# Optimization experiments

Measured on AMD Instinct MI355X. Metric: run time of the kernel, lower is better.

## Reference

```python
import jax, jax.numpy as jnp
import numpy as np

N, F, H, K, O = 16384, 64, 128, 16, 10


def setup_inputs() -> dict:
    key = jax.random.key(0)
    ks = jax.random.split(key, 12)
    s = lambda fan: 1.0 / np.sqrt(fan)
    return {
        "x": jax.random.normal(ks[0], (N, F), dtype=jnp.float32),
        "edge_index": jax.random.randint(ks[1], (2, N * 8), 0, N),  # unused by forward
        "mlp_w1": jax.random.normal(ks[2], (2 * F, H), dtype=jnp.float32) * s(2 * F),
        "mlp_b1": jnp.zeros((H,), jnp.float32),
        "mlp_w2": jax.random.normal(ks[3], (H, H), dtype=jnp.float32) * s(H),
        "mlp_b2": jnp.zeros((H,), jnp.float32),
        "gcn_w": jax.random.normal(ks[4], (H, H), dtype=jnp.float32) * s(H),
        "gcn_b": jnp.zeros((H,), jnp.float32),
        "gnn_out_w": jax.random.normal(ks[5], (H, H), dtype=jnp.float32) * s(H),
        "gnn_out_b": jnp.zeros((H,), jnp.float32),
        "out_w": jax.random.normal(ks[6], (H, O), dtype=jnp.float32) * s(H),
        "out_b": jnp.zeros((O,), jnp.float32),
        "k": K,
    }


def _forward(x, mlp_w1, mlp_b1, mlp_w2, mlp_b2, gcn_w, gcn_b,
             gnn_out_w, gnn_out_b, out_w, out_b, k):
    n = x.shape[0]
    # ---- dynamic kNN graph in feature space (includes self, dist 0) ----
    sq = jnp.sum(x * x, axis=-1)                       # [N]
    d2 = sq[:, None] + sq[None, :] - 2.0 * (x @ x.T)   # [N,N] squared dists
    _, idx = jax.lax.top_k(-d2, k)                     # [N,k] neighbor (source) ids per query
    # ---- EdgeConv message: MLP(cat(x_i, x_j - x_i)), max-aggregate over k ----
    x_j = x[idx]                                       # [N,k,F]
    x_i = jnp.broadcast_to(x[:, None, :], x_j.shape)   # [N,k,F]
    m = jnp.concatenate([x_i, x_j - x_i], axis=-1)     # [N,k,2F]
    m = jax.nn.relu(m @ mlp_w1 + mlp_b1)
    m = jax.nn.log_softmax(m @ mlp_w2 + mlp_b2, axis=-1)
    h = jnp.max(m, axis=1)                             # [N,H] max aggregation
    # ---- GCNConv on the kNN edge_index (+ self loops, symmetric norm) ----
    loop = jnp.arange(n)
    src = jnp.concatenate([idx.reshape(-1), loop])     # sources (x_j)
    dst = jnp.concatenate([jnp.repeat(loop, k), loop]) # targets (x_i)
    deg = jax.ops.segment_sum(jnp.ones_like(src, h.dtype), dst, num_segments=n)
    dinv = jax.lax.rsqrt(jnp.maximum(deg, 1.0))
    norm = dinv[src] * dinv[dst]                       # [E]
    hw = h @ gcn_w                                     # [N,H]
    h = jax.ops.segment_sum(norm[:, None] * hw[src], dst, num_segments=n) + gcn_b
    # ---- inner GNN output head (Linear + Softmax) ----
    h = jax.nn.softmax(h @ gnn_out_w + gnn_out_b, axis=-1)
    # ---- GNN_Combo output head (Linear + Softmax) ----
    return jax.nn.softmax(h @ out_w + out_b, axis=-1)  # [N,O]


def reference(x, edge_index, mlp_w1, mlp_b1, mlp_w2, mlp_b2, gcn_w, gcn_b,
              gnn_out_w, gnn_out_b, out_w, out_b, k):
    # edge_index is accepted by GNN_Combo.forward but unused (kNN graph replaces it)
    del edge_index
    return _forward(x, mlp_w1, mlp_b1, mlp_w2, mlp_b2, gcn_w, gcn_b,
                    gnn_out_w, gnn_out_b, out_w, out_b, k)
```

## Files before the change

kernel.cpp:

```cpp
#include <hip/hip_runtime.h>
#include <hip/hip_fp16.h>
#include <cfloat>
#include <cmath>
#include <string.h>


#define N_NODES 16384
#define F_IN    64
#define H_DIM   128
#define K_NN    16
#define O_DIM   10

typedef _Float16 half8  __attribute__((ext_vector_type(8)));
typedef _Float16 half4v __attribute__((ext_vector_type(4)));
typedef _Float16 half2v __attribute__((ext_vector_type(2)));
typedef __fp16   fp16x2 __attribute__((ext_vector_type(2)));
typedef float    floatx4 __attribute__((ext_vector_type(4)));

__device__ __forceinline__ void async_copy16(void* lds, const void* g) {
  __builtin_amdgcn_global_load_lds(
      (const __attribute__((address_space(1))) unsigned int*)g,
      (__attribute__((address_space(3))) unsigned int*)lds, 16, 0, 0);
}

__device__ __forceinline__ unsigned pack2h(float a, float b) {
  half2v p; p[0] = (_Float16)a; p[1] = (_Float16)b;
  unsigned u; __builtin_memcpy(&u, &p, 4); return u;
}
__device__ __forceinline__ float unpacklo(unsigned u) {
  half2v p; __builtin_memcpy(&p, &u, 4); return (float)p[0];
}
__device__ __forceinline__ float unpackhi(unsigned u) {
  half2v p; __builtin_memcpy(&p, &u, 4); return (float)p[1];
}
__device__ __forceinline__ fp16x2 as_h2(unsigned u) {
  fp16x2 p; __builtin_memcpy(&p, &u, 4); return p;
}

__global__ __launch_bounds__(256) void k_prep(const float* __restrict__ x,
                                              float* __restrict__ sq,
                                              double* __restrict__ sq64,
                                              _Float16* __restrict__ xh,
                                              unsigned* __restrict__ cnt) {
  const int i = blockIdx.x * 256 + threadIdx.x;
  if (i >= N_NODES) return;
  const float4* r = (const float4*)(x + i * F_IN);
  float s = 0.f; double sd = 0.0;
#pragma unroll
  for (int q = 0; q < 16; ++q) {
    const float4 v = r[q];
    s += v.x*v.x + v.y*v.y + v.z*v.z + v.w*v.w;
    sd += (double)v.x*v.x + (double)v.y*v.y + (double)v.z*v.z + (double)v.w*v.w;
    half4v hv;
    hv[0] = (_Float16)v.x; hv[1] = (_Float16)v.y;
    hv[2] = (_Float16)v.z; hv[3] = (_Float16)v.w;
    *(half4v*)(xh + (size_t)i * F_IN + 4 * q) = hv;
  }
  sq[i] = s; sq64[i] = sd; cnt[i] = 0;
}

__global__ __launch_bounds__(256) void k_gemm(const _Float16* __restrict__ xh,
                                              const float* __restrict__ sq,
                                              char* __restrict__ subg) {
  __shared__ __align__(16) _Float16 stage[128 * 64];
  __shared__ float sqs[128];
  const int tid = threadIdx.x;
  const int wv = tid >> 6, l = tid & 63;
  const int lane16 = l & 15, quad = l >> 4;
  const int rowblk = (blockIdx.x >> 5) * 256;
  const int seg = blockIdx.x & 31;
  const int rw = rowblk + wv * 64;

  half8 B[4][2];
#pragma unroll
  for (int s = 0; s < 4; ++s) {
    const _Float16* bp = xh + (size_t)(rw + s * 16 + lane16) * F_IN + quad * 8;
    B[s][0] = *(const half8*)(bp);
    B[s][1] = *(const half8*)(bp + 32);
  }

  const int lcol8 = l >> 3;
  const int lchk  = (l & 7) ^ lcol8;
  const size_t lgoff = (size_t)lcol8 * F_IN + lchk * 8;

  unsigned sel[16];

#pragma unroll
  for (int tile = 0; tile < 4; ++tile) {
    const int c0 = seg * 512 + tile * 128;
    __syncthreads();
    if (tid < 128) sqs[tid] = sq[c0 + tid];
#pragma unroll
    for (int q = 0; q < 4; ++q) {
      const int grp = wv * 4 + q;
      async_copy16(stage + grp * 512,
                   xh + (size_t)(c0 + grp * 8) * F_IN + lgoff);
    }
    __syncthreads();

    float sprev[4];
    unsigned pk[4][4];
#pragma unroll
    for (int st = 0; st < 8; ++st) {
      const _Float16* base = stage + (st * 16 + lane16) * 64;
      const int sw = lane16 & 7;
      const half8 A0 = *(const half8*)(base + ((quad ^ sw) * 8));
      const half8 A1 = *(const half8*)(base + (((4 + quad) ^ sw) * 8));
      const floatx4 sq4 = *(const floatx4*)(sqs + st * 16 + quad * 4);
      floatx4 acc[4];
#pragma unroll
      for (int s = 0; s < 4; ++s) acc[s] = (floatx4)0.f;
#pragma unroll
      for (int s = 0; s < 4; ++s)
        acc[s] = __builtin_amdgcn_mfma_f32_16x16x32_f16(A0, B[s][0], acc[s], 0, 0, 0);
#pragma unroll
      for (int s = 0; s < 4; ++s)
        acc[s] = __builtin_amdgcn_mfma_f32_16x16x32_f16(A1, B[s][1], acc[s], 0, 0, 0);
#pragma unroll
      for (int s = 0; s < 4; ++s) {
        const float k0 = fmaf(-2.f, acc[s][0], sq4[0]);
        const float k1 = fmaf(-2.f, acc[s][1], sq4[1]);
        const float k2 = fmaf(-2.f, acc[s][2], sq4[2]);
        const float k3 = fmaf(-2.f, acc[s][3], sq4[3]);
        float m = fminf(fminf(k0, k1), fminf(k2, k3));
        m = fminf(m, __shfl_xor(m, 16, 64));
        m = fminf(m, __shfl_xor(m, 32, 64));
        if ((st & 1) == 0) sprev[s] = m;
        else pk[s][st >> 1] = pack2h(sprev[s], m);
      }
    }
#pragma unroll
    for (int t = 0; t < 4; ++t) {
      unsigned o = pk[0][t];
      if (quad == 1) o = pk[1][t];
      if (quad == 2) o = pk[2][t];
      if (quad == 3) o = pk[3][t];
      sel[tile * 4 + t] = o;
    }
  }
  __syncthreads();
  {
    unsigned* sc = (unsigned*)stage + wv * 1024;
#pragma unroll
    for (int k = 0; k < 16; ++k) sc[k * 64 + l] = sel[k];
    char* dstw = subg + ((size_t)seg * N_NODES + rw) * 64;
#pragma unroll
    for (int t = 0; t < 4; ++t) {
      const int rl = t * 16 + (l >> 2);
      uint4 ov;
      ov.x = sc[((l & 3) * 4 + 0) * 64 + rl];
      ov.y = sc[((l & 3) * 4 + 1) * 64 + rl];
      ov.z = sc[((l & 3) * 4 + 2) * 64 + rl];
      ov.w = sc[((l & 3) * 4 + 3) * 64 + rl];
      *(uint4*)(dstw + t * 1024 + l * 16) = ov;
    }
  }
}

__global__ __launch_bounds__(256) void k_filter(const _Float16* __restrict__ xh,
                                                const float* __restrict__ sq,
                                                const char* __restrict__ subg,
                                                unsigned* __restrict__ cnt,
                                                int* __restrict__ cand) {
  const int l = threadIdx.x & 63;
  const int i = blockIdx.x * 4 + (threadIdx.x >> 6);
  const int part = l & 3, c = l >> 2;

  fp16x2 xi2[8];
  {
    const uint4* xp = (const uint4*)(xh + (size_t)i * F_IN + part * 16);
    const uint4 a = xp[0], b = xp[1];
    xi2[0] = as_h2(a.x); xi2[1] = as_h2(a.y); xi2[2] = as_h2(a.z); xi2[3] = as_h2(a.w);
    xi2[4] = as_h2(b.x); xi2[5] = as_h2(b.y); xi2[6] = as_h2(b.z); xi2[7] = as_h2(b.w);
  }
  float subs[16];
  {
    const char* sp = subg + ((size_t)(l >> 1) * N_NODES + i) * 64 + (l & 1) * 32;
    const uint4 a = *(const uint4*)(sp);
    const uint4 b = *(const uint4*)(sp + 16);
    subs[0] = unpacklo(a.x); subs[1] = unpackhi(a.x);
    subs[2] = unpacklo(a.y); subs[3] = unpackhi(a.y);
    subs[4] = unpacklo(a.z); subs[5] = unpackhi(a.z);
    subs[6] = unpacklo(a.w); subs[7] = unpackhi(a.w);
    subs[8] = unpacklo(b.x); subs[9] = unpackhi(b.x);
    subs[10] = unpacklo(b.y); subs[11] = unpackhi(b.y);
    subs[12] = unpacklo(b.z); subs[13] = unpackhi(b.z);
    subs[14] = unpacklo(b.w); subs[15] = unpackhi(b.w);
  }
  float cmin = subs[0];
#pragma unroll
  for (int t = 1; t < 16; ++t) cmin = fminf(cmin, subs[t]);
  int rank = 0;
#pragma unroll 4
  for (int j = 0; j < 64; ++j) {
    const float vj = __shfl(cmin, j, 64);
    rank += (vj < cmin) || (vj == cmin && j < l);
  }
  const unsigned long long rm = __ballot(rank == 15);
  const int srcl = __ffsll((long long)rm) - 1;
  const float thr = __shfl(cmin, srcl, 64) + 0.25f;

  unsigned selmask = 0;
#pragma unroll
  for (int t = 0; t < 16; ++t) selmask |= (subs[t] <= thr) ? (1u << t) : 0u;

  unsigned long long act;
  while ((act = __ballot(selmask != 0)) != 0ull) {
    const int src = __ffsll((long long)act) - 1;
    unsigned m = __shfl(selmask, src, 64);
    if (l == src) selmask = 0;
    while (m) {
      const int b = __ffs(m) - 1; m &= m - 1;
      const int sid = src * 16 + b;
      const int cg = sid * 16 + c;
      float d = 0.f;
      {
        const uint4* gp = (const uint4*)(xh + (size_t)cg * F_IN + part * 16);
        const uint4 g0 = gp[0], g1 = gp[1];
        d = __builtin_amdgcn_fdot2(xi2[0], as_h2(g0.x), d, false);
        d = __builtin_amdgcn_fdot2(xi2[1], as_h2(g0.y), d, false);
        d = __builtin_amdgcn_fdot2(xi2[2], as_h2(g0.z), d, false);
        d = __builtin_amdgcn_fdot2(xi2[3], as_h2(g0.w), d, false);
        d = __builtin_amdgcn_fdot2(xi2[4], as_h2(g1.x), d, false);
        d = __builtin_amdgcn_fdot2(xi2[5], as_h2(g1.y), d, false);
        d = __builtin_amdgcn_fdot2(xi2[6], as_h2(g1.z), d, false);
        d = __builtin_amdgcn_fdot2(xi2[7], as_h2(g1.w), d, false);
      }
      d += __shfl_xor(d, 1, 64);
      d += __shfl_xor(d, 2, 64);
      const float key = fmaf(-2.f, d, sq[cg]);
      const bool pred = (part == 0) && (key <= thr);
      const unsigned long long am = __ballot(pred);
      if (am) {
        const int ldr = __ffsll((long long)am) - 1;
        unsigned base = 0;
        if (l == ldr) base = atomicAdd(&cnt[i], (unsigned)__popcll(am));
        base = __shfl(base, ldr, 64);
        if (pred) {
          const unsigned idx = base + (unsigned)__popcll(am & ((1ull << l) - 1ull));
          if (idx < 128u) cand[(size_t)i * 128 + idx] = cg;
        }
      }
    }
  }
}

__global__ __launch_bounds__(128) void k_rescore(const float* __restrict__ x,
                                                 const double* __restrict__ sq64,
                                                 const int* __restrict__ cand,
                                                 const unsigned* __restrict__ cnt,
                                                 int* __restrict__ knn) {
  __shared__ float  xi[F_IN];
  __shared__ double keys[128];
  __shared__ int    ids[128];
  const int i = blockIdx.x, t = threadIdx.x;
  const unsigned cv = cnt[i];
  const int n = (int)(cv < 128u ? cv : 128u);
  if (t < F_IN) xi[t] = x[i * F_IN + t];
  __syncthreads();
  double key = 1e300; int id = 0x7fffffff;
  if (t < n) {
    id = cand[(size_t)i * 128 + t];
    const float4* xc4 = (const float4*)(x + (size_t)id * F_IN);
    double d0 = 0.0, d1 = 0.0, d2 = 0.0, d3 = 0.0;
#pragma unroll
    for (int q = 0; q < 16; ++q) {
      const float4 v = xc4[q];
      d0 += (double)xi[4*q+0] * (double)v.x;
      d1 += (double)xi[4*q+1] * (double)v.y;
      d2 += (double)xi[4*q+2] * (double)v.z;
      d3 += (double)xi[4*q+3] * (double)v.w;
    }
    key = sq64[id] - 2.0 * ((d0 + d1) + (d2 + d3));
  }
  keys[t] = key; ids[t] = id;
  __syncthreads();
  int rank = 0;
  for (int cix = 0; cix < n; ++cix) {
    const double kc = keys[cix]; const int ic = ids[cix];
    rank += (kc < key) || (kc == key && ic < id);
  }
  if (t < n && rank < K_NN) knn[i * K_NN + rank] = id;
}

__global__ __launch_bounds__(256, 2) void k_lin12(const float* __restrict__ x,
                                                  const float* __restrict__ w1,
                                                  const float* __restrict__ b1,
                                                  _Float16* __restrict__ Ph,
                                                  _Float16* __restrict__ Qh) {
  __shared__ float wl[2 * F_IN][H_DIM];
  for (int s = threadIdx.x; s < 2 * F_IN * H_DIM; s += 256) wl[s >> 7][s & 127] = w1[s];
  __syncthreads();
  const int node = blockIdx.x * 32 + (threadIdx.x & 31);
  const int ob = (threadIdx.x >> 5) * 16;
  float accR[16], accQ[16];
#pragma unroll
  for (int o = 0; o < 16; ++o) { accR[o] = 0.f; accQ[o] = 0.f; }
  const float4* xr = (const float4*)(x + node * F_IN);
#define L1STEP(ff, xs) { \
    const float* wt_ = &wl[(ff)][ob]; \
    const float* wb_ = &wl[(ff) + F_IN][ob]; \
    _Pragma("unroll") \
    for (int o = 0; o < 16; o += 4) { \
      const float4 t4 = *(const float4*)(wt_ + o); \
      const float4 b4 = *(const float4*)(wb_ + o); \
      accR[o+0] = fmaf((xs), t4.x, accR[o+0]); accQ[o+0] = fmaf((xs), b4.x, accQ[o+0]); \
      accR[o+1] = fmaf((xs), t4.y, accR[o+1]); accQ[o+1] = fmaf((xs), b4.y, accQ[o+1]); \
      accR[o+2] = fmaf((xs), t4.z, accR[o+2]); accQ[o+2] = fmaf((xs), b4.z, accQ[o+2]); \
      accR[o+3] = fmaf((xs), t4.w, accR[o+3]); accQ[o+3] = fmaf((xs), b4.w, accQ[o+3]); } }
#pragma unroll 2
  for (int q = 0; q < 16; ++q) {
    const float4 xv = xr[q];
    L1STEP(4*q+0, xv.x); L1STEP(4*q+1, xv.y); L1STEP(4*q+2, xv.z); L1STEP(4*q+3, xv.w);
  }
#undef L1STEP
  _Float16* pp = Ph + (size_t)node * H_DIM + ob;
  _Float16* qp = Qh + (size_t)node * H_DIM + ob;
#pragma unroll
  for (int o = 0; o < 16; o += 4) {
    half4v hp, hq;
#pragma unroll
    for (int u = 0; u < 4; ++u) {
      hp[u] = (_Float16)(accR[o+u] - accQ[o+u] + b1[ob + o + u]);
      hq[u] = (_Float16)accQ[o+u];
    }
    *(half4v*)(pp + o) = hp;
    *(half4v*)(qp + o) = hq;
  }
}

__global__ __launch_bounds__(256, 2) void k_edgeconv(const _Float16* __restrict__ Ph,
                                                     const _Float16* __restrict__ Qh,
                                                     const float* __restrict__ w2,
                                                     const float* __restrict__ b2,
                                                     const int* __restrict__ knn,
                                                     float* __restrict__ h) {
  __shared__ __align__(16) _Float16 wt[H_DIM * 128];
  __shared__ __align__(16) _Float16 afr[4][2048];
  const int tid = threadIdx.x;
  const int wv = tid >> 6, l = tid & 63;
  const int lane16 = l & 15, quad = l >> 4;

  {
    const int n = tid >> 1, part = tid & 1;
    const float* wsrc = w2 + n;
    _Float16* wdst = wt + n * 128;
#pragma unroll
    for (int c = 0; c < 8; ++c) {
      half8 hv;
#pragma unroll
      for (int u = 0; u < 8; ++u)
        hv[u] = (_Float16)wsrc[(size_t)(part * 64 + c * 8 + u) * H_DIM];
      *(half8*)(wdst + (((part * 8 + c) ^ (n & 15)) * 8)) = hv;
    }
  }
  __syncthreads();

  float b2r[8];
#pragma unroll
  for (int tile = 0; tile < 8; ++tile) b2r[tile] = b2[tile * 16 + lane16];

  const int i0 = blockIdx.x * 32 + wv * 8;
  int js[8];
#pragma unroll
  for (int it = 0; it < 8; ++it) js[it] = knn[(i0 + it) * K_NN + lane16];

  _Float16* aw = afr[wv];
  half8 pc[4], qc[4];
  {
    const half8* pr = (const half8*)(Ph + (size_t)i0 * H_DIM + quad * 32);
    const half8* qr = (const half8*)(Qh + (size_t)js[0] * H_DIM + quad * 32);
#pragma unroll
    for (int c = 0; c < 4; ++c) { pc[c] = pr[c]; qc[c] = qr[c]; }
  }
  for (int it = 0; it < 8; ++it) {
    const int i = i0 + it;
    half8 pn[4], qn[4];
    if (it < 7) {
      const half8* pr = (const half8*)(Ph + (size_t)(i + 1) * H_DIM + quad * 32);
      const half8* qr = (const half8*)(Qh + (size_t)js[it + 1] * H_DIM + quad * 32);
#pragma unroll
      for (int c = 0; c < 4; ++c) { pn[c] = pr[c]; qn[c] = qr[c]; }
    }
#pragma unroll
    for (int c = 0; c < 4; ++c) {
      half8 z = pc[c] + qc[c];
      half8 r;
#pragma unroll
      for (int u = 0; u < 8; ++u) r[u] = z[u] > (_Float16)0 ? z[u] : (_Float16)0;
      *(half8*)(aw + quad * 512 + c * 128 + lane16 * 8) = r;
    }
    half8 A[4];
#pragma unroll
    for (int kb = 0; kb < 4; ++kb) A[kb] = *(const half8*)(aw + kb * 512 + l * 8);
    floatx4 acc[8];
#pragma unroll
    for (int tile = 0; tile < 8; ++tile) acc[tile] = (floatx4)0.f;
#pragma unroll
    for (int kb = 0; kb < 4; ++kb) {
#pragma unroll
      for (int tile = 0; tile < 8; ++tile) {
        const half8 B = *(const half8*)(wt + (tile * 16 + lane16) * 128 +
                                        (((kb * 4 + quad) ^ lane16) * 8));
        acc[tile] = __builtin_amdgcn_mfma_f32_16x16x32_f16(A[kb], B, acc[tile], 0, 0, 0);
      }
    }
    float lse[4];
#pragma unroll
    for (int r = 0; r < 4; ++r) {
      float mx = acc[0][r] + b2r[0];
#pragma unroll
      for (int tile = 1; tile < 8; ++tile) mx = fmaxf(mx, acc[tile][r] + b2r[tile]);
      mx = fmaxf(mx, __shfl_xor(mx, 1, 64));
      mx = fmaxf(mx, __shfl_xor(mx, 2, 64));
      mx = fmaxf(mx, __shfl_xor(mx, 4, 64));
      mx = fmaxf(mx, __shfl_xor(mx, 8, 64));
      float e = 0.f;
#pragma unroll
      for (int tile = 0; tile < 8; ++tile) e += __expf(acc[tile][r] + b2r[tile] - mx);
      e += __shfl_xor(e, 1, 64);
      e += __shfl_xor(e, 2, 64);
      e += __shfl_xor(e, 4, 64);
      e += __shfl_xor(e, 8, 64);
      lse[r] = mx + __logf(e);
    }
#pragma unroll
    for (int tile = 0; tile < 8; ++tile) {
      float v = acc[tile][0] + b2r[tile] - lse[0];
#pragma unroll
      for (int r = 1; r < 4; ++r) v = fmaxf(v, acc[tile][r] + b2r[tile] - lse[r]);
      v = fmaxf(v, __shfl_xor(v, 16, 64));
      v = fmaxf(v, __shfl_xor(v, 32, 64));
      if (quad == 0) h[(size_t)i * H_DIM + tile * 16 + lane16] = v;
    }
#pragma unroll
    for (int c = 0; c < 4; ++c) { pc[c] = pn[c]; qc[c] = qn[c]; }
  }
}

__global__ __launch_bounds__(256) void k_hw(const float* __restrict__ h,
                                            const float* __restrict__ gw,
                                            _Float16* __restrict__ hwh) {
  __shared__ float wl[H_DIM][H_DIM];
  for (int s = threadIdx.x; s < H_DIM * H_DIM; s += 256) wl[s >> 7][s & 127] = gw[s];
  __syncthreads();
  const int node = blockIdx.x * 32 + (threadIdx.x & 31);
  const int ob = (threadIdx.x >> 5) * 16;
  float acc[16];
#pragma unroll
  for (int o = 0; o < 16; ++o) acc[o] = 0.f;
  const float4* hr = (const float4*)(h + node * H_DIM);
#define HWSTEP(ff, xs) { \
    const float* wr = &wl[(ff)][ob]; \
    _Pragma("unroll") \
    for (int o = 0; o < 16; o += 4) { const float4 w4 = *(const float4*)(wr + o); \
      acc[o+0] = fmaf((xs), w4.x, acc[o+0]); \
      acc[o+1] = fmaf((xs), w4.y, acc[o+1]); \
      acc[o+2] = fmaf((xs), w4.z, acc[o+2]); \
      acc[o+3] = fmaf((xs), w4.w, acc[o+3]); } }
#pragma unroll 2
  for (int q = 0; q < 32; ++q) {
    const float4 hv = hr[q];
    HWSTEP(4*q+0, hv.x); HWSTEP(4*q+1, hv.y); HWSTEP(4*q+2, hv.z); HWSTEP(4*q+3, hv.w);
  }
#undef HWSTEP
  _Float16* dp = hwh + (size_t)node * H_DIM + ob;
#pragma unroll
  for (int o = 0; o < 16; o += 4) {
    half4v hv;
#pragma unroll
    for (int u = 0; u < 4; ++u) hv[u] = (_Float16)acc[o + u];
    *(half4v*)(dp + o) = hv;
  }
}

__global__ __launch_bounds__(256) void k_heads(const _Float16* __restrict__ hwh,
                                               const int* __restrict__ knn,
                                               const float* __restrict__ gb,
                                               const float* __restrict__ gow,
                                               const float* __restrict__ gob,
                                               const float* __restrict__ ow,
                                               const float* __restrict__ obv,
                                               float* __restrict__ out) {
  __shared__ unsigned int wgo[H_DIM][64];
  __shared__ float hbuf[4][H_DIM];
  for (int s = threadIdx.x; s < H_DIM * 64; s += 256) {
    const int f = s >> 6, l = s & 63;
    wgo[f][l] = pack2h(gow[f * H_DIM + 2 * l], gow[f * H_DIM + 2 * l + 1]);
  }
  __syncthreads();
  const int wv = threadIdx.x >> 6, l = threadIdx.x & 63;
  const unsigned* hw32 = (const unsigned*)hwh;
  const float gbl = gb[2 * l], gbh = gb[2 * l + 1];
  const float gobl = gob[2 * l], gobh = gob[2 * l + 1];
  for (int it = 0; it < 8; ++it) {
    const int i = blockIdx.x * 32 + wv * 8 + it;
    const int* kr = knn + i * K_NN;
    unsigned u = hw32[(size_t)i * 64 + l];
    float s0 = unpacklo(u), s1 = unpackhi(u);
#pragma unroll
    for (int m = 0; m < K_NN; ++m) {
      const unsigned um = hw32[(size_t)kr[m] * 64 + l];
      s0 += unpacklo(um);
      s1 += unpackhi(um);
    }
    const float hg0 = s0 * (1.0f / 17.0f) + gbl;
    const float hg1 = s1 * (1.0f / 17.0f) + gbh;
    hbuf[wv][2 * l] = hg0; hbuf[wv][2 * l + 1] = hg1;
    float z0 = gobl, z1 = gobh;
#pragma unroll 4
    for (int f = 0; f < H_DIM; ++f) {
      const float hv = hbuf[wv][f];
      const unsigned int wvv = wgo[f][l];
      z0 = fmaf(hv, unpacklo(wvv), z0);
      z1 = fmaf(hv, unpackhi(wvv), z1);
    }
    float mx = fmaxf(z0, z1);
#pragma unroll
    for (int s = 1; s < 64; s <<= 1) mx = fmaxf(mx, __shfl_xor(mx, s, 64));
    const float e0 = __expf(z0 - mx), e1 = __expf(z1 - mx);
    float sm = e0 + e1;
#pragma unroll
    for (int s = 1; s < 64; s <<= 1) sm += __shfl_xor(sm, s, 64);
    const float h20 = e0 / sm, h21 = e1 / sm;
    float zc[O_DIM];
#pragma unroll
    for (int c = 0; c < O_DIM; ++c) {
      float a = h20 * ow[(2 * l) * O_DIM + c] + h21 * ow[(2 * l + 1) * O_DIM + c];
#pragma unroll
      for (int s = 1; s < 64; s <<= 1) a += __shfl_xor(a, s, 64);
      zc[c] = a + obv[c];
    }
    float m10 = zc[0];
#pragma unroll
    for (int c = 1; c < O_DIM; ++c) m10 = fmaxf(m10, zc[c]);
    float es[O_DIM]; float s10 = 0.f;
#pragma unroll
    for (int c = 0; c < O_DIM; ++c) { es[c] = __expf(zc[c] - m10); s10 += es[c]; }
    const float inv = 1.0f / s10;
    if (l < O_DIM) {
      float v = es[0];
#pragma unroll
      for (int c = 1; c < O_DIM; ++c) if (l == c) v = es[c];
      out[i * O_DIM + l] = v * inv;
    }
  }
}

extern "C" void kernel_launch(void* const* d_in, const int* in_sizes, int n_in,
                              void* d_out, int out_size, void* d_ws, size_t ws_size,
                              hipStream_t stream) {
  (void)in_sizes; (void)n_in; (void)out_size; (void)ws_size;
  const float* x   = (const float*)d_in[0];
  const float* w1  = (const float*)d_in[2];
  const float* b1  = (const float*)d_in[3];
  const float* w2  = (const float*)d_in[4];
  const float* b2  = (const float*)d_in[5];
  const float* gw  = (const float*)d_in[6];
  const float* gb  = (const float*)d_in[7];
  const float* gow = (const float*)d_in[8];
  const float* gob = (const float*)d_in[9];
  const float* ow  = (const float*)d_in[10];
  const float* obv = (const float*)d_in[11];
  float* out = (float*)d_out;

  char* ws = (char*)d_ws;
  constexpr size_t MB = 1024 * 1024;
  constexpr size_t OFF_SQ   = 0;
  constexpr size_t OFF_SQ64 = OFF_SQ   + (size_t)N_NODES * 4;
  constexpr size_t OFF_XH   = OFF_SQ64 + (size_t)N_NODES * 8;
  constexpr size_t OFF_CNT  = OFF_XH   + (size_t)N_NODES * F_IN * 2;
  constexpr size_t OFF_CAND = OFF_CNT  + (size_t)N_NODES * 4;
  constexpr size_t OFF_SUBG = OFF_CAND + (size_t)N_NODES * 128 * 4;
  constexpr size_t OFF_KNN  = OFF_SUBG;
  constexpr size_t OFF_H    = OFF_SUBG + 1 * MB;
  constexpr size_t OFF_HWH  = OFF_SUBG + 9 * MB;
  float*     sq   = (float*)    (ws + OFF_SQ);
  double*    sq64 = (double*)   (ws + OFF_SQ64);
  _Float16*  xh   = (_Float16*) (ws + OFF_XH);
  unsigned*  cnt  = (unsigned*) (ws + OFF_CNT);
  int*       cand = (int*)      (ws + OFF_CAND);
  char*      subg = (char*)     (ws + OFF_SUBG);
  int*       knn  = (int*)      (ws + OFF_KNN);
  float*     h    = (float*)    (ws + OFF_H);
  _Float16*  hwh  = (_Float16*) (ws + OFF_HWH);
  _Float16*  Ph   = (_Float16*) (ws + OFF_CAND);
  _Float16*  Qh   = (_Float16*) (ws + OFF_CAND + 4 * MB);

  k_prep    <<<N_NODES / 256, 256, 0, stream>>>(x, sq, sq64, xh, cnt);
  k_gemm    <<<2048,          256, 0, stream>>>(xh, sq, subg);
  k_filter  <<<N_NODES / 4,   256, 0, stream>>>(xh, sq, subg, cnt, cand);
  k_rescore <<<N_NODES,       128, 0, stream>>>(x, sq64, cand, cnt, knn);
  k_lin12   <<<N_NODES / 32,  256, 0, stream>>>(x, w1, b1, Ph, Qh);
  k_edgeconv<<<N_NODES / 32,  256, 0, stream>>>(Ph, Qh, w2, b2, knn, h);
  k_hw      <<<N_NODES / 32,  256, 0, stream>>>(h, gw, hwh);
  k_heads   <<<N_NODES / 32,  256, 0, stream>>>(hwh, knn, gb, gow, gob, ow, obv, out);
}
```

Before: 331.5 us.

## Fuse kNN rescoring into filter kernel with LDS candidate lists and prefetch

Merges the filter and double-precision rescore kernels into one kernel. Candidate sub-groups go into a per-wave LDS list instead of global cand/cnt buffers, and the next candidate group's rows are software-prefetched. The GEMM also folds the -2 scale into B and seeds the accumulator with sq, which removes the per-element fma. This saves a kernel launch, global candidate traffic and the counter reset, but caps the sub-group list at 160 entries and adds block-wide syncs across four independent waves.

```diff
diff --git a/kernel.cpp b/kernel.cpp
--- a/kernel.cpp
+++ b/kernel.cpp
@@ -40,8 +40,7 @@
 __global__ __launch_bounds__(256) void k_prep(const float* __restrict__ x,
                                               float* __restrict__ sq,
                                               double* __restrict__ sq64,
-                                              _Float16* __restrict__ xh,
-                                              unsigned* __restrict__ cnt) {
+                                              _Float16* __restrict__ xh) {
   const int i = blockIdx.x * 256 + threadIdx.x;
   if (i >= N_NODES) return;
   const float4* r = (const float4*)(x + i * F_IN);
@@ -56,7 +55,7 @@
     hv[2] = (_Float16)v.z; hv[3] = (_Float16)v.w;
     *(half4v*)(xh + (size_t)i * F_IN + 4 * q) = hv;
   }
-  sq[i] = s; sq64[i] = sd; cnt[i] = 0;
+  sq[i] = s; sq64[i] = sd;
 }
 
 __global__ __launch_bounds__(256) void k_gemm(const _Float16* __restrict__ xh,
@@ -72,11 +71,14 @@
   const int rw = rowblk + wv * 64;
 
   half8 B[4][2];
+  half8 neg2;
+#pragma unroll
+  for (int u = 0; u < 8; ++u) neg2[u] = (_Float16)(-2.0f);
 #pragma unroll
   for (int s = 0; s < 4; ++s) {
     const _Float16* bp = xh + (size_t)(rw + s * 16 + lane16) * F_IN + quad * 8;
-    B[s][0] = *(const half8*)(bp);
-    B[s][1] = *(const half8*)(bp + 32);
+    B[s][0] = *(const half8*)(bp) * neg2;
+    B[s][1] = *(const half8*)(bp + 32) * neg2;
   }
 
   const int lcol8 = l >> 3;
@@ -109,7 +111,7 @@
       const floatx4 sq4 = *(const floatx4*)(sqs + st * 16 + quad * 4);
       floatx4 acc[4];
 #pragma unroll
-      for (int s = 0; s < 4; ++s) acc[s] = (floatx4)0.f;
+      for (int s = 0; s < 4; ++s) acc[s] = sq4;
 #pragma unroll
       for (int s = 0; s < 4; ++s)
         acc[s] = __builtin_amdgcn_mfma_f32_16x16x32_f16(A0, B[s][0], acc[s], 0, 0, 0);
@@ -118,11 +120,7 @@
         acc[s] = __builtin_amdgcn_mfma_f32_16x16x32_f16(A1, B[s][1], acc[s], 0, 0, 0);
 #pragma unroll
       for (int s = 0; s < 4; ++s) {
-        const float k0 = fmaf(-2.f, acc[s][0], sq4[0]);
-        const float k1 = fmaf(-2.f, acc[s][1], sq4[1]);
-        const float k2 = fmaf(-2.f, acc[s][2], sq4[2]);
-        const float k3 = fmaf(-2.f, acc[s][3], sq4[3]);
-        float m = fminf(fminf(k0, k1), fminf(k2, k3));
+        float m = fminf(fminf(acc[s][0], acc[s][1]), fminf(acc[s][2], acc[s][3]));
         m = fminf(m, __shfl_xor(m, 16, 64));
         m = fminf(m, __shfl_xor(m, 32, 64));
         if ((st & 1) == 0) sprev[s] = m;
@@ -160,10 +158,18 @@
 __global__ __launch_bounds__(256) void k_filter(const _Float16* __restrict__ xh,
                                                 const float* __restrict__ sq,
                                                 const char* __restrict__ subg,
-                                                unsigned* __restrict__ cnt,
-                                                int* __restrict__ cand) {
+                                                const float* __restrict__ x,
+                                                const double* __restrict__ sq64,
+                                                int* __restrict__ knn) {
+  __shared__ int    list[4][160];
+  __shared__ int    wcnt[4];
+  __shared__ int    clist[4][128];
+  __shared__ int    ccnt[4];
+  __shared__ double kbuf[4][128];
+  __shared__ float  xbuf[4][F_IN];
   const int l = threadIdx.x & 63;
-  const int i = blockIdx.x * 4 + (threadIdx.x >> 6);
+  const int wv = threadIdx.x >> 6;
+  const int i = blockIdx.x * 4 + wv;
   const int part = l & 3, c = l >> 2;
 
   fp16x2 xi2[8];
@@ -204,83 +210,90 @@
 #pragma unroll
   for (int t = 0; t < 16; ++t) selmask |= (subs[t] <= thr) ? (1u << t) : 0u;
 
-  unsigned long long act;
-  while ((act = __ballot(selmask != 0)) != 0ull) {
-    const int src = __ffsll((long long)act) - 1;
-    unsigned m = __shfl(selmask, src, 64);
-    if (l == src) selmask = 0;
+  if (l == 0) { wcnt[wv] = 0; ccnt[wv] = 0; }
+  __syncthreads();
+  int base = 0;
+  if (selmask) base = atomicAdd(&wcnt[wv], __popc(selmask));
+  {
+    unsigned m = selmask; int idx = base;
     while (m) {
       const int b = __ffs(m) - 1; m &= m - 1;
-      const int sid = src * 16 + b;
-      const int cg = sid * 16 + c;
-      float d = 0.f;
-      {
-        const uint4* gp = (const uint4*)(xh + (size_t)cg * F_IN + part * 16);
-        const uint4 g0 = gp[0], g1 = gp[1];
-        d = __builtin_amdgcn_fdot2(xi2[0], as_h2(g0.x), d, false);
-        d = __builtin_amdgcn_fdot2(xi2[1], as_h2(g0.y), d, false);
-        d = __builtin_amdgcn_fdot2(xi2[2], as_h2(g0.z), d, false);
-        d = __builtin_amdgcn_fdot2(xi2[3], as_h2(g0.w), d, false);
-        d = __builtin_amdgcn_fdot2(xi2[4], as_h2(g1.x), d, false);
-        d = __builtin_amdgcn_fdot2(xi2[5], as_h2(g1.y), d, false);
-        d = __builtin_amdgcn_fdot2(xi2[6], as_h2(g1.z), d, false);
-        d = __builtin_amdgcn_fdot2(xi2[7], as_h2(g1.w), d, false);
+      if (idx < 160) list[wv][idx] = l * 16 + b;
+      ++idx;
+    }
+  }
+  __syncthreads();
+  int n = wcnt[wv]; if (n > 160) n = 160;
+
+  uint4 g0a, g0b, g1a, g1b;
+  int colc = 0, coln = 0;
+  if (n > 0) {
+    colc = list[wv][0] * 16;
+    const uint4* gp = (const uint4*)(xh + (size_t)(colc + c) * F_IN + part * 16);
+    g0a = gp[0]; g0b = gp[1];
+  }
+  for (int j = 0; j < n; ++j) {
+    if (j + 1 < n) {
+      coln = list[wv][j + 1] * 16;
+      const uint4* gp = (const uint4*)(xh + (size_t)(coln + c) * F_IN + part * 16);
+      g1a = gp[0]; g1b = gp[1];
+    }
+    float d = 0.f;
+    d = __builtin_amdgcn_fdot2(xi2[0], as_h2(g0a.x), d, false);
+    d = __builtin_amdgcn_fdot2(xi2[1], as_h2(g0a.y), d, false);
+    d = __builtin_amdgcn_fdot2(xi2[2], as_h2(g0a.z), d, false);
+    d = __builtin_amdgcn_fdot2(xi2[3], as_h2(g0a.w), d, false);
+    d = __builtin_amdgcn_fdot2(xi2[4], as_h2(g0b.x), d, false);
+    d = __builtin_amdgcn_fdot2(xi2[5], as_h2(g0b.y), d, false);
+    d = __builtin_amdgcn_fdot2(xi2[6], as_h2(g0b.z), d, false);
+    d = __builtin_amdgcn_fdot2(xi2[7], as_h2(g0b.w), d, false);
+    d += __shfl_xor(d, 1, 64);
+    d += __shfl_xor(d, 2, 64);
+    const int cg = colc + c;
+    const float key = fmaf(-2.f, d, sq[cg]);
+    const bool pred = (part == 0) && (key <= thr);
+    const unsigned long long am = __ballot(pred);
+    if (am) {
+      const int ldr = __ffsll((long long)am) - 1;
+      int cb = 0;
+      if (l == ldr) cb = atomicAdd(&ccnt[wv], (int)__popcll(am));
+      cb = __shfl(cb, ldr, 64);
+      if (pred) {
+        const int idx = cb + (int)__popcll(am & ((1ull << l) - 1ull));
+        if (idx < 128) clist[wv][idx] = cg;
       }
-      d += __shfl_xor(d, 1, 64);
-      d += __shfl_xor(d, 2, 64);
-      const float key = fmaf(-2.f, d, sq[cg]);
-      const bool pred = (part == 0) && (key <= thr);
-      const unsigned long long am = __ballot(pred);
-      if (am) {
-        const int ldr = __ffsll((long long)am) - 1;
-        unsigned base = 0;
-        if (l == ldr) base = atomicAdd(&cnt[i], (unsigned)__popcll(am));
-        base = __shfl(base, ldr, 64);
-        if (pred) {
-          const unsigned idx = base + (unsigned)__popcll(am & ((1ull << l) - 1ull));
-          if (idx < 128u) cand[(size_t)i * 128 + idx] = cg;
-        }
-      }
-    }
-  }
-}
-
-__global__ __launch_bounds__(128) void k_rescore(const float* __restrict__ x,
-                                                 const double* __restrict__ sq64,
-                                                 const int* __restrict__ cand,
-                                                 const unsigned* __restrict__ cnt,
-                                                 int* __restrict__ knn) {
-  __shared__ float  xi[F_IN];
-  __shared__ double keys[128];
-  __shared__ int    ids[128];
-  const int i = blockIdx.x, t = threadIdx.x;
-  const unsigned cv = cnt[i];
-  const int n = (int)(cv < 128u ? cv : 128u);
-  if (t < F_IN) xi[t] = x[i * F_IN + t];
-  __syncthreads();
-  double key = 1e300; int id = 0x7fffffff;
-  if (t < n) {
-    id = cand[(size_t)i * 128 + t];
+    }
+    colc = coln;
+    g0a = g1a; g0b = g1b;
+  }
+  xbuf[wv][l] = x[(size_t)i * F_IN + l];
+  __syncthreads();
+
+  int n2 = ccnt[wv]; if (n2 > 128) n2 = 128;
+  for (int j = l; j < n2; j += 64) {
+    const int id = clist[wv][j];
     const float4* xc4 = (const float4*)(x + (size_t)id * F_IN);
     double d0 = 0.0, d1 = 0.0, d2 = 0.0, d3 = 0.0;
 #pragma unroll
     for (int q = 0; q < 16; ++q) {
       const float4 v = xc4[q];
-      d0 += (double)xi[4*q+0] * (double)v.x;
-      d1 += (double)xi[4*q+1] * (double)v.y;
-      d2 += (double)xi[4*q+2] * (double)v.z;
-      d3 += (double)xi[4*q+3] * (double)v.w;
-    }
-    key = sq64[id] - 2.0 * ((d0 + d1) + (d2 + d3));
-  }
-  keys[t] = key; ids[t] = id;
-  __syncthreads();
-  int rank = 0;
-  for (int cix = 0; cix < n; ++cix) {
-    const double kc = keys[cix]; const int ic = ids[cix];
-    rank += (kc < key) || (kc == key && ic < id);
-  }
-  if (t < n && rank < K_NN) knn[i * K_NN + rank] = id;
+      d0 += (double)xbuf[wv][4*q+0] * (double)v.x;
+      d1 += (double)xbuf[wv][4*q+1] * (double)v.y;
+      d2 += (double)xbuf[wv][4*q+2] * (double)v.z;
+      d3 += (double)xbuf[wv][4*q+3] * (double)v.w;
+    }
+    kbuf[wv][j] = sq64[id] - 2.0 * ((d0 + d1) + (d2 + d3));
+  }
+  __syncthreads();
+  for (int j = l; j < n2; j += 64) {
+    const double kj = kbuf[wv][j]; const int idj = clist[wv][j];
+    int rk = 0;
+    for (int t = 0; t < n2; ++t) {
+      const double kt = kbuf[wv][t]; const int it = clist[wv][t];
+      rk += (kt < kj) || (kt == kj && it < idj);
+    }
+    if (rk < K_NN) knn[i * K_NN + rk] = idj;
+  }
 }
 
 __global__ __launch_bounds__(256, 2) void k_lin12(const float* __restrict__ x,
@@ -569,28 +582,24 @@
   constexpr size_t OFF_SQ   = 0;
   constexpr size_t OFF_SQ64 = OFF_SQ   + (size_t)N_NODES * 4;
   constexpr size_t OFF_XH   = OFF_SQ64 + (size_t)N_NODES * 8;
-  constexpr size_t OFF_CNT  = OFF_XH   + (size_t)N_NODES * F_IN * 2;
-  constexpr size_t OFF_CAND = OFF_CNT  + (size_t)N_NODES * 4;
-  constexpr size_t OFF_SUBG = OFF_CAND + (size_t)N_NODES * 128 * 4;
+  constexpr size_t OFF_PQ   = OFF_XH   + (size_t)N_NODES * F_IN * 2;
+  constexpr size_t OFF_SUBG = OFF_PQ   + 8 * MB;
   constexpr size_t OFF_KNN  = OFF_SUBG;
   constexpr size_t OFF_H    = OFF_SUBG + 1 * MB;
   constexpr size_t OFF_HWH  = OFF_SUBG + 9 * MB;
   float*     sq   = (float*)    (ws + OFF_SQ);
   double*    sq64 = (double*)   (ws + OFF_SQ64);
   _Float16*  xh   = (_Float16*) (ws + OFF_XH);
-  unsigned*  cnt  = (unsigned*) (ws + OFF_CNT);
-  int*       cand = (int*)      (ws + OFF_CAND);
   char*      subg = (char*)     (ws + OFF_SUBG);
   int*       knn  = (int*)      (ws + OFF_KNN);
   float*     h    = (float*)    (ws + OFF_H);
   _Float16*  hwh  = (_Float16*) (ws + OFF_HWH);
-  _Float16*  Ph   = (_Float16*) (ws + OFF_CAND);
-  _Float16*  Qh   = (_Float16*) (ws + OFF_CAND + 4 * MB);
-
-  k_prep    <<<N_NODES / 256, 256, 0, stream>>>(x, sq, sq64, xh, cnt);
+  _Float16*  Ph   = (_Float16*) (ws + OFF_PQ);
+  _Float16*  Qh   = (_Float16*) (ws + OFF_PQ + 4 * MB);
+
+  k_prep    <<<N_NODES / 256, 256, 0, stream>>>(x, sq, sq64, xh);
   k_gemm    <<<2048,          256, 0, stream>>>(xh, sq, subg);
-  k_filter  <<<N_NODES / 4,   256, 0, stream>>>(xh, sq, subg, cnt, cand);
-  k_rescore <<<N_NODES,       128, 0, stream>>>(x, sq64, cand, cnt, knn);
+  k_filter  <<<N_NODES / 4,   256, 0, stream>>>(xh, sq, subg, x, sq64, knn);
   k_lin12   <<<N_NODES / 32,  256, 0, stream>>>(x, w1, b1, Ph, Qh);
   k_edgeconv<<<N_NODES / 32,  256, 0, stream>>>(Ph, Qh, w2, b2, knn, h);
   k_hw      <<<N_NODES / 32,  256, 0, stream>>>(h, gw, hwh);
```

Result: slower. 358.3 us (+8.1%).
